# Kernel optimization log

Hardware: AMD Instinct MI355X
Metric: run time of the kernel (lower is better)

## Reference

```python
import jax, jax.numpy as jnp
import numpy as np

B, H, T, K, V = 2, 8, 2048, 128, 128


def setup_inputs() -> dict:
    key = jax.random.key(0)
    k1, k2, k3, k4, k5 = jax.random.split(key, 5)
    return {
        "q": jax.random.normal(k1, (B, H, T, K), dtype=jnp.float32),
        "k": jax.random.normal(k2, (B, H, T, K), dtype=jnp.float32),
        "v": jax.random.normal(k3, (B, H, T, V), dtype=jnp.float32),
        "i_gate": jax.random.normal(k4, (B, H, T), dtype=jnp.float32),
        "f_gate": jax.random.normal(k5, (B, H, T), dtype=jnp.float32),
    }


def reference(q, k, v, i_gate, f_gate):
    # Stabilized parallel mLSTM (same math as the chunked Triton kernel,
    # expressed in natural-log base instead of base-2).
    Bq, Hq, Tq, Kd = q.shape
    scale = Kd ** -0.5
    logf = jax.nn.log_sigmoid(f_gate)                      # [B,H,T]
    fc = jnp.cumsum(logf, axis=-1)                         # cumulative forget logits
    # log decay matrix: logD[t,s] = i[s] + (fc[t] - fc[s]) for s <= t
    logD = fc[..., :, None] - fc[..., None, :] + i_gate[..., None, :]  # [B,H,T,T]
    mask = jnp.tril(jnp.ones((Tq, Tq), dtype=bool))
    logD_masked = jnp.where(mask, logD, -jnp.inf)
    m = jnp.max(logD_masked, axis=-1)                      # row-wise stabilizer [B,H,T]
    D = jnp.where(mask, jnp.exp(logD - m[..., None]), 0.0) # stabilized decay matrix
    S = jnp.einsum("bhtk,bhsk->bhts", q, k) * scale * D    # gated scores
    norm = jnp.maximum(jnp.abs(jnp.sum(S, axis=-1)), jnp.exp(-m))  # [B,H,T]
    h = jnp.einsum("bhts,bhsv->bhtv", S, v) / norm[..., None]
    return h
```

## Files before the change

kernel.cpp:

```cpp
#include <hip/hip_runtime.h>

#define T_SEQ 2048
#define DHEAD 128
#define NBH 16
#define SCALE 0.08838834764831845f

typedef unsigned short u16;
typedef u16 u16x4 __attribute__((ext_vector_type(4)));
typedef u16 u16x8 __attribute__((ext_vector_type(8)));
typedef __bf16 bf16x8 __attribute__((ext_vector_type(8)));
typedef float f32x4 __attribute__((ext_vector_type(4)));

__device__ __forceinline__ u16 f2bfu(float x) {
  union { float f; unsigned u; } c; c.f = x;
  unsigned u = c.u;
  u = u + 0x7FFFu + ((u >> 16) & 1u);
  return (u16)(u >> 16);
}

__device__ __forceinline__ bf16x8 ldsFrag(const u16* p) {
  u16x8 t = *(const u16x8*)p;
  return __builtin_bit_cast(bf16x8, t);
}

__device__ __forceinline__ void gld_lds16(const void* g, void* l) {
  __builtin_amdgcn_global_load_lds(
      (__attribute__((address_space(1))) const unsigned int*)g,
      (__attribute__((address_space(3))) unsigned int*)l, 16, 0, 0);
}

__global__ __launch_bounds__(256) void gate_scan_kernel(
    const float* __restrict__ ig, const float* __restrict__ fg,
    float* __restrict__ a_out, float* __restrict__ c_out,
    float* __restrict__ nfl_out)
{
  const int bh  = blockIdx.x;
  const int tid = threadIdx.x;
  const int base = bh * T_SEQ + tid * 8;
  __shared__ float sbuf[256];

  float lf[8];
  float run = 0.f;
#pragma unroll
  for (int j = 0; j < 8; ++j) {
    float x  = fg[base + j];
    float ls = fminf(x, 0.f) - log1pf(expf(-fabsf(x)));
    run += ls; lf[j] = run;
  }
  sbuf[tid] = run; __syncthreads();
  for (int off = 1; off < 256; off <<= 1) {
    float t = (tid >= off) ? sbuf[tid - off] : 0.f;
    __syncthreads();
    sbuf[tid] += t;
    __syncthreads();
  }
  const float excl = (tid > 0) ? sbuf[tid - 1] : 0.f;
  __syncthreads();

  float fc[8], cm[8];
  float runm = -INFINITY;
#pragma unroll
  for (int j = 0; j < 8; ++j) {
    fc[j] = excl + lf[j];
    float av = ig[base + j] - fc[j];
    a_out[base + j] = av;
    runm = fmaxf(runm, av);
    cm[j] = runm;
  }
  sbuf[tid] = runm; __syncthreads();
  for (int off = 1; off < 256; off <<= 1) {
    float t = (tid >= off) ? sbuf[tid - off] : -INFINITY;
    __syncthreads();
    sbuf[tid] = fmaxf(sbuf[tid], t);
    __syncthreads();
  }
  const float exclm = (tid > 0) ? sbuf[tid - 1] : -INFINITY;
#pragma unroll
  for (int j = 0; j < 8; ++j) {
    float c = fmaxf(exclm, cm[j]);
    c_out[base + j]   = c;
    nfl_out[base + j] = expf(-(c + fc[j]));
  }
}

__global__ __launch_bounds__(256) void cvt_k_kernel(
    const float* __restrict__ src, u16* __restrict__ dst)
{
  const int i = (blockIdx.x * 256 + threadIdx.x) * 4;
  const float4 x = *(const float4*)(src + i);
  u16x4 p; p[0] = f2bfu(x.x); p[1] = f2bfu(x.y); p[2] = f2bfu(x.z); p[3] = f2bfu(x.w);
  *(u16x4*)(dst + i) = p;
}

__global__ __launch_bounds__(256) void cvt_vt_kernel(
    const float* __restrict__ v, u16* __restrict__ vt)
{
  const int bh = blockIdx.y, kt = blockIdx.x, tid = threadIdx.x;
  __shared__ __align__(16) u16 L[128 * 72];
  const int n0 = (tid & 31) * 4, k0 = (tid >> 5) * 8;
  const float* vp = v + ((size_t)bh * T_SEQ + kt * 64 + k0) * DHEAD + n0;
  u16 tv[4][8];
#pragma unroll
  for (int rr = 0; rr < 8; ++rr) {
    const float4 x = *(const float4*)(vp + rr * DHEAD);
    tv[0][rr] = f2bfu(x.x); tv[1][rr] = f2bfu(x.y);
    tv[2][rr] = f2bfu(x.z); tv[3][rr] = f2bfu(x.w);
  }
#pragma unroll
  for (int j = 0; j < 4; ++j) {
    u16x8 p;
#pragma unroll
    for (int rr = 0; rr < 8; ++rr) p[rr] = tv[j][rr];
    *(u16x8*)(&L[(n0 + j) * 72 + k0]) = p;
  }
  __syncthreads();
  const int row = tid >> 1, s0 = (tid & 1) * 32;
  u16* op = vt + ((size_t)bh * DHEAD + row) * T_SEQ + kt * 64 + s0;
#pragma unroll
  for (int i = 0; i < 4; ++i)
    *(u16x8*)(op + i * 8) = *(const u16x8*)(&L[row * 72 + s0 + i * 8]);
}

template <bool FAST>
__global__ __launch_bounds__(256, 2) void mlstm_fwd_kernel(
    const float* __restrict__ qg, const float* __restrict__ kg,
    const float* __restrict__ vg,
    const u16* __restrict__ kbf, const u16* __restrict__ vtbf,
    const float* __restrict__ ag, const float* __restrict__ cg,
    const float* __restrict__ nflg, float* __restrict__ out)
{
  const int bx = (int)blockIdx.x;
  const int xs = bx & 7, js = bx >> 3;
  const int bh = xs + 8 * (js & 1);
  const int qt = 31 - (js >> 1);

  const int tid  = (int)threadIdx.x;
  const int wave = tid >> 6, lane = tid & 63;
  const int quad = lane >> 4, l16 = lane & 15;

  __shared__ __align__(16) u16 KB[2][64 * 128];
  __shared__ __align__(16) u16 VB[2][128 * 64];
  __shared__ __align__(16) u16 Pl[4][16 * 72];

  const size_t hoff = (size_t)bh * T_SEQ * DHEAD;
  const int goff = bh * T_SEQ;
  const int qrowA = qt * 64 + wave * 16 + l16;
  const int trow0 = qt * 64 + wave * 16 + quad * 4;

  bf16x8 qf[4];
  {
    const float* qp = qg + hoff + (size_t)qrowA * DHEAD + quad * 8;
#pragma unroll
    for (int kc = 0; kc < 4; ++kc) {
      const float4 x0 = *(const float4*)(qp + kc * 32);
      const float4 x1 = *(const float4*)(qp + kc * 32 + 4);
      u16x8 t;
      t[0] = f2bfu(x0.x); t[1] = f2bfu(x0.y); t[2] = f2bfu(x0.z); t[3] = f2bfu(x0.w);
      t[4] = f2bfu(x1.x); t[5] = f2bfu(x1.y); t[6] = f2bfu(x1.z); t[7] = f2bfu(x1.w);
      qf[kc] = __builtin_bit_cast(bf16x8, t);
    }
  }
  float cr[4];
#pragma unroll
  for (int r = 0; r < 4; ++r) cr[r] = cg[goff + trow0 + r];

  f32x4 oa[8];
#pragma unroll
  for (int nv = 0; nv < 8; ++nv) oa[nv] = (f32x4){0.f, 0.f, 0.f, 0.f};
  float rs[4] = {0.f, 0.f, 0.f, 0.f};

  float4 kr[8], vr[8];
  const int fb_keyb = tid >> 4;
  const int fb_db   = (tid & 15) ^ ((tid >> 4) & 7);
  const int fb_n0 = (tid & 31) * 4, fb_k0 = (tid >> 5) * 8;

  auto stage_issue = [&](int kt, int b) {
    if (FAST) {
      const u16* ks = kbf + ((size_t)goff + kt * 64) * DHEAD;
      const u16* vs = vtbf + (size_t)bh * DHEAD * T_SEQ + kt * 64;
#pragma unroll
      for (int j = 0; j < 4; ++j) {
        const int B = (wave * 4 + j) * 64 + lane;
        {
          const int key = B >> 4;
          const int db = (B & 15) ^ (key & 7);
          gld_lds16(ks + (size_t)key * DHEAD + db * 8, &KB[b][(wave * 4 + j) * 512]);
        }
        {
          const int n = B >> 3;
          const int kb = (B & 7) ^ (n & 7);
          gld_lds16(vs + (size_t)n * T_SEQ + kb * 8, &VB[b][(wave * 4 + j) * 512]);
        }
      }
    } else {
      const float* kp = kg + hoff + (size_t)(kt * 64) * DHEAD;
      const float* vp = vg + hoff + (size_t)(kt * 64 + fb_k0) * DHEAD + fb_n0;
#pragma unroll
      for (int jb = 0; jb < 4; ++jb) {
        const int key = fb_keyb + 16 * jb;
        kr[2 * jb]     = *(const float4*)(kp + (size_t)key * DHEAD + fb_db * 8);
        kr[2 * jb + 1] = *(const float4*)(kp + (size_t)key * DHEAD + fb_db * 8 + 4);
      }
#pragma unroll
      for (int rr = 0; rr < 8; ++rr) vr[rr] = *(const float4*)(vp + rr * DHEAD);
    }
  };
  auto stage_commit = [&](int b) {
    if (!FAST) {
#pragma unroll
      for (int jb = 0; jb < 4; ++jb) {
        const int key = fb_keyb + 16 * jb;
        u16x8 p;
        p[0] = f2bfu(kr[2*jb].x);   p[1] = f2bfu(kr[2*jb].y);
        p[2] = f2bfu(kr[2*jb].z);   p[3] = f2bfu(kr[2*jb].w);
        p[4] = f2bfu(kr[2*jb+1].x); p[5] = f2bfu(kr[2*jb+1].y);
        p[6] = f2bfu(kr[2*jb+1].z); p[7] = f2bfu(kr[2*jb+1].w);
        *(u16x8*)(&KB[b][(key * 16 + (tid & 15)) * 8]) = p;
      }
      u16 tv[4][8];
#pragma unroll
      for (int rr = 0; rr < 8; ++rr) {
        tv[0][rr] = f2bfu(vr[rr].x); tv[1][rr] = f2bfu(vr[rr].y);
        tv[2][rr] = f2bfu(vr[rr].z); tv[3][rr] = f2bfu(vr[rr].w);
      }
      const int kb = fb_k0 >> 3;
#pragma unroll
      for (int j = 0; j < 4; ++j) {
        const int n = fb_n0 + j;
        u16x8 p;
#pragma unroll
        for (int rr = 0; rr < 8; ++rr) p[rr] = tv[j][rr];
        *(u16x8*)(&VB[b][(n * 8 + (kb ^ (n & 7))) * 8]) = p;
      }
    }
  };

  stage_issue(0, 0);
  stage_commit(0);
  __syncthreads();

  for (int kt = 0; kt <= qt; ++kt) {
    const int b = kt & 1;
    if (kt < qt) stage_issue(kt + 1, b ^ 1);

    float an[4];
#pragma unroll
    for (int nc = 0; nc < 4; ++nc) an[nc] = ag[goff + kt * 64 + nc * 16 + l16];

    const bool diag = (kt == qt);
#pragma unroll
    for (int nc = 0; nc < 4; ++nc) {
      f32x4 s = (f32x4){0.f, 0.f, 0.f, 0.f};
      const int key = nc * 16 + l16;
#pragma unroll
      for (int kc = 0; kc < 4; ++kc) {
        const int db = (kc * 4 + quad) ^ (l16 & 7);
        const bf16x8 bk = ldsFrag(&KB[b][(key * 16 + db) * 8]);
        s = __builtin_amdgcn_mfma_f32_16x16x32_bf16(qf[kc], bk, s, 0, 0, 0);
      }
      const float asv = an[nc];
      const int scol = nc * 16 + l16;
#pragma unroll
      for (int r = 0; r < 4; ++r) {
        float p = s[r] * (SCALE * __expf(asv - cr[r]));
        if (diag && (kt * 64 + scol > trow0 + r)) p = 0.f;
        rs[r] += p;
        Pl[wave][(quad * 4 + r) * 72 + scol] = f2bfu(p);
      }
    }
#pragma unroll
    for (int kk = 0; kk < 2; ++kk) {
      const bf16x8 pa = ldsFrag(&Pl[wave][l16 * 72 + kk * 32 + quad * 8]);
#pragma unroll
      for (int nv = 0; nv < 8; ++nv) {
        const int n = nv * 16 + l16;
        const int kb = (kk * 4 + quad) ^ (l16 & 7);
        const bf16x8 bv = ldsFrag(&VB[b][(n * 8 + kb) * 8]);
        oa[nv] = __builtin_amdgcn_mfma_f32_16x16x32_bf16(pa, bv, oa[nv], 0, 0, 0);
      }
    }
    if (kt < qt) stage_commit(b ^ 1);
    __syncthreads();
  }

#pragma unroll
  for (int r = 0; r < 4; ++r) {
    float x = rs[r];
#pragma unroll
    for (int off = 1; off < 16; off <<= 1) x += __shfl_xor(x, off, 64);
    rs[r] = x;
  }
  float inv[4];
#pragma unroll
  for (int r = 0; r < 4; ++r) {
    const float nf = nflg[goff + trow0 + r];
    inv[r] = 1.f / fmaxf(fabsf(rs[r]), nf);
  }
  float* op = out + hoff;
#pragma unroll
  for (int nv = 0; nv < 8; ++nv) {
#pragma unroll
    for (int r = 0; r < 4; ++r) {
      op[(size_t)(trow0 + r) * DHEAD + nv * 16 + l16] = oa[nv][r] * inv[r];
    }
  }
}

extern "C" void kernel_launch(void* const* d_in, const int* in_sizes, int n_in,
                              void* d_out, int out_size, void* d_ws, size_t ws_size,
                              hipStream_t stream) {
  const float* q  = (const float*)d_in[0];
  const float* k  = (const float*)d_in[1];
  const float* v  = (const float*)d_in[2];
  const float* ig = (const float*)d_in[3];
  const float* fg = (const float*)d_in[4];

  const size_t gate_bytes = (size_t)3 * NBH * T_SEQ * sizeof(float);
  const size_t kv_elems   = (size_t)NBH * T_SEQ * DHEAD;
  const bool fast = ws_size >= gate_bytes + 2 * kv_elems * sizeof(u16);

  float* a_ws   = (float*)d_ws;
  float* c_ws   = a_ws + NBH * T_SEQ;
  float* nfl_ws = c_ws + NBH * T_SEQ;
  u16* kbf  = (u16*)((char*)d_ws + gate_bytes);
  u16* vtbf = kbf + kv_elems;

  gate_scan_kernel<<<dim3(NBH), dim3(256), 0, stream>>>(ig, fg, a_ws, c_ws, nfl_ws);
  if (fast) {
    cvt_k_kernel<<<dim3((unsigned)(kv_elems / 1024)), dim3(256), 0, stream>>>(k, kbf);
    cvt_vt_kernel<<<dim3(T_SEQ / 64, NBH), dim3(256), 0, stream>>>(v, vtbf);
    mlstm_fwd_kernel<true><<<dim3(512), dim3(256), 0, stream>>>(
        q, k, v, kbf, vtbf, a_ws, c_ws, nfl_ws, (float*)d_out);
  } else {
    mlstm_fwd_kernel<false><<<dim3(512), dim3(256), 0, stream>>>(
        q, k, v, kbf, vtbf, a_ws, c_ws, nfl_ws, (float*)d_out);
  }
}
```

Measured before the change: 154.5 us.

## Pair complementary query tiles per block and hoist exp stabilizer per tile

Each 512-thread block now handles two query tiles of the same head, p and 31-p, in two 256-thread groups. This gives every block the same causal work, and the 256-block grid can place one block per CU. The per-element exp(a - c_row) is replaced by a per-column exp(a - c_tile) and a per-row correction at the end, which cuts exponentials in the inner loop. The P scratch tile gets an XOR swizzle to reduce LDS bank conflicts. Costs: the two groups load K/V separately, so traffic is duplicated, and the shorter group idles at barriers until the longer one finishes. The new stabilization also carries some overflow and precision risk.

Result: slower. 158.0 us (+2.2%).

```diff
diff --git a/kernel.cpp b/kernel.cpp
--- a/kernel.cpp
+++ b/kernel.cpp
@@ -122,7 +122,7 @@
 }
 
 template <bool FAST>
-__global__ __launch_bounds__(256, 2) void mlstm_fwd_kernel(
+__global__ __launch_bounds__(512, 1) void mlstm_fwd_kernel(
     const float* __restrict__ qg, const float* __restrict__ kg,
     const float* __restrict__ vg,
     const u16* __restrict__ kbf, const u16* __restrict__ vtbf,
@@ -130,17 +130,20 @@
     const float* __restrict__ nflg, float* __restrict__ out)
 {
   const int bx = (int)blockIdx.x;
-  const int xs = bx & 7, js = bx >> 3;
-  const int bh = xs + 8 * (js & 1);
-  const int qt = 31 - (js >> 1);
-
-  const int tid  = (int)threadIdx.x;
-  const int wave = tid >> 6, lane = tid & 63;
+  const int bh = bx & 15, p = bx >> 4;
+  const int tid = (int)threadIdx.x;
+  const int grp = tid >> 8;
+  const int gt  = tid & 255;
+  const int wave = gt >> 6, lane = gt & 63;
   const int quad = lane >> 4, l16 = lane & 15;
-
-  __shared__ __align__(16) u16 KB[2][64 * 128];
-  __shared__ __align__(16) u16 VB[2][128 * 64];
-  __shared__ __align__(16) u16 Pl[4][16 * 72];
+  const int w8   = tid >> 6;
+
+  const int qt    = grp ? p : (31 - p);
+  const int qtMax = 31 - p;
+
+  __shared__ __align__(16) u16 KB[2][2][64 * 128];
+  __shared__ __align__(16) u16 VB[2][2][128 * 64];
+  __shared__ __align__(16) u16 Pl[8][16 * 64];
 
   const size_t hoff = (size_t)bh * T_SEQ * DHEAD;
   const int goff = bh * T_SEQ;
@@ -160,9 +163,7 @@
       qf[kc] = __builtin_bit_cast(bf16x8, t);
     }
   }
-  float cr[4];
-#pragma unroll
-  for (int r = 0; r < 4; ++r) cr[r] = cg[goff + trow0 + r];
+  const float cmax = cg[goff + qt * 64 + 63];
 
   f32x4 oa[8];
 #pragma unroll
@@ -170,9 +171,9 @@
   float rs[4] = {0.f, 0.f, 0.f, 0.f};
 
   float4 kr[8], vr[8];
-  const int fb_keyb = tid >> 4;
-  const int fb_db   = (tid & 15) ^ ((tid >> 4) & 7);
-  const int fb_n0 = (tid & 31) * 4, fb_k0 = (tid >> 5) * 8;
+  const int fb_keyb = gt >> 4;
+  const int fb_db   = (gt & 15) ^ ((gt >> 4) & 7);
+  const int fb_n0 = (gt & 31) * 4, fb_k0 = (gt >> 5) * 8;
 
   auto stage_issue = [&](int kt, int b) {
     if (FAST) {
@@ -184,12 +185,12 @@
         {
           const int key = B >> 4;
           const int db = (B & 15) ^ (key & 7);
-          gld_lds16(ks + (size_t)key * DHEAD + db * 8, &KB[b][(wave * 4 + j) * 512]);
+          gld_lds16(ks + (size_t)key * DHEAD + db * 8, &KB[grp][b][(wave * 4 + j) * 512]);
         }
         {
           const int n = B >> 3;
           const int kb = (B & 7) ^ (n & 7);
-          gld_lds16(vs + (size_t)n * T_SEQ + kb * 8, &VB[b][(wave * 4 + j) * 512]);
+          gld_lds16(vs + (size_t)n * T_SEQ + kb * 8, &VB[grp][b][(wave * 4 + j) * 512]);
         }
       }
     } else {
@@ -210,12 +211,12 @@
 #pragma unroll
       for (int jb = 0; jb < 4; ++jb) {
         const int key = fb_keyb + 16 * jb;
-        u16x8 p;
-        p[0] = f2bfu(kr[2*jb].x);   p[1] = f2bfu(kr[2*jb].y);
-        p[2] = f2bfu(kr[2*jb].z);   p[3] = f2bfu(kr[2*jb].w);
-        p[4] = f2bfu(kr[2*jb+1].x); p[5] = f2bfu(kr[2*jb+1].y);
-        p[6] = f2bfu(kr[2*jb+1].z); p[7] = f2bfu(kr[2*jb+1].w);
-        *(u16x8*)(&KB[b][(key * 16 + (tid & 15)) * 8]) = p;
+        u16x8 pk;
+        pk[0] = f2bfu(kr[2*jb].x);   pk[1] = f2bfu(kr[2*jb].y);
+        pk[2] = f2bfu(kr[2*jb].z);   pk[3] = f2bfu(kr[2*jb].w);
+        pk[4] = f2bfu(kr[2*jb+1].x); pk[5] = f2bfu(kr[2*jb+1].y);
+        pk[6] = f2bfu(kr[2*jb+1].z); pk[7] = f2bfu(kr[2*jb+1].w);
+        *(u16x8*)(&KB[grp][b][(key * 16 + (gt & 15)) * 8]) = pk;
       }
       u16 tv[4][8];
 #pragma unroll
@@ -227,10 +228,10 @@
 #pragma unroll
       for (int j = 0; j < 4; ++j) {
         const int n = fb_n0 + j;
-        u16x8 p;
-#pragma unroll
-        for (int rr = 0; rr < 8; ++rr) p[rr] = tv[j][rr];
-        *(u16x8*)(&VB[b][(n * 8 + (kb ^ (n & 7))) * 8]) = p;
+        u16x8 pk;
+#pragma unroll
+        for (int rr = 0; rr < 8; ++rr) pk[rr] = tv[j][rr];
+        *(u16x8*)(&VB[grp][b][(n * 8 + (kb ^ (n & 7))) * 8]) = pk;
       }
     }
   };
@@ -239,47 +240,51 @@
   stage_commit(0);
   __syncthreads();
 
-  for (int kt = 0; kt <= qt; ++kt) {
+  for (int kt = 0; kt <= qtMax; ++kt) {
     const int b = kt & 1;
-    if (kt < qt) stage_issue(kt + 1, b ^ 1);
-
-    float an[4];
-#pragma unroll
-    for (int nc = 0; nc < 4; ++nc) an[nc] = ag[goff + kt * 64 + nc * 16 + l16];
-
-    const bool diag = (kt == qt);
-#pragma unroll
-    for (int nc = 0; nc < 4; ++nc) {
-      f32x4 s = (f32x4){0.f, 0.f, 0.f, 0.f};
-      const int key = nc * 16 + l16;
-#pragma unroll
-      for (int kc = 0; kc < 4; ++kc) {
-        const int db = (kc * 4 + quad) ^ (l16 & 7);
-        const bf16x8 bk = ldsFrag(&KB[b][(key * 16 + db) * 8]);
-        s = __builtin_amdgcn_mfma_f32_16x16x32_bf16(qf[kc], bk, s, 0, 0, 0);
-      }
-      const float asv = an[nc];
-      const int scol = nc * 16 + l16;
-#pragma unroll
-      for (int r = 0; r < 4; ++r) {
-        float p = s[r] * (SCALE * __expf(asv - cr[r]));
-        if (diag && (kt * 64 + scol > trow0 + r)) p = 0.f;
-        rs[r] += p;
-        Pl[wave][(quad * 4 + r) * 72 + scol] = f2bfu(p);
-      }
-    }
-#pragma unroll
-    for (int kk = 0; kk < 2; ++kk) {
-      const bf16x8 pa = ldsFrag(&Pl[wave][l16 * 72 + kk * 32 + quad * 8]);
-#pragma unroll
-      for (int nv = 0; nv < 8; ++nv) {
-        const int n = nv * 16 + l16;
-        const int kb = (kk * 4 + quad) ^ (l16 & 7);
-        const bf16x8 bv = ldsFrag(&VB[b][(n * 8 + kb) * 8]);
-        oa[nv] = __builtin_amdgcn_mfma_f32_16x16x32_bf16(pa, bv, oa[nv], 0, 0, 0);
-      }
-    }
-    if (kt < qt) stage_commit(b ^ 1);
+    const bool act = (kt <= qt);
+    if (act && kt < qt) stage_issue(kt + 1, b ^ 1);
+
+    if (act) {
+      float an[4];
+#pragma unroll
+      for (int nc = 0; nc < 4; ++nc) an[nc] = ag[goff + kt * 64 + nc * 16 + l16];
+
+      const bool diag = (kt == qt);
+#pragma unroll
+      for (int nc = 0; nc < 4; ++nc) {
+        f32x4 s = (f32x4){0.f, 0.f, 0.f, 0.f};
+        const int key = nc * 16 + l16;
+#pragma unroll
+        for (int kc = 0; kc < 4; ++kc) {
+          const int db = (kc * 4 + quad) ^ (l16 & 7);
+          const bf16x8 bk = ldsFrag(&KB[grp][b][(key * 16 + db) * 8]);
+          s = __builtin_amdgcn_mfma_f32_16x16x32_bf16(qf[kc], bk, s, 0, 0, 0);
+        }
+        const float es = SCALE * __expf(an[nc] - cmax);
+        const int scol = nc * 16 + l16;
+#pragma unroll
+        for (int r = 0; r < 4; ++r) {
+          float pv = s[r] * es;
+          if (diag && (kt * 64 + scol > trow0 + r)) pv = 0.f;
+          rs[r] += pv;
+          const int m = quad * 4 + r;
+          Pl[w8][m * 64 + ((((scol >> 3) ^ (m & 7)) << 3) | (scol & 7))] = f2bfu(pv);
+        }
+      }
+#pragma unroll
+      for (int kk = 0; kk < 2; ++kk) {
+        const bf16x8 pa = ldsFrag(&Pl[w8][l16 * 64 + (((kk * 4 + quad) ^ (l16 & 7)) << 3)]);
+#pragma unroll
+        for (int nv = 0; nv < 8; ++nv) {
+          const int n = nv * 16 + l16;
+          const int kb = (kk * 4 + quad) ^ (l16 & 7);
+          const bf16x8 bv = ldsFrag(&VB[grp][b][(n * 8 + kb) * 8]);
+          oa[nv] = __builtin_amdgcn_mfma_f32_16x16x32_bf16(pa, bv, oa[nv], 0, 0, 0);
+        }
+      }
+    }
+    if (act && kt < qt) stage_commit(b ^ 1);
     __syncthreads();
   }
 
@@ -293,8 +298,10 @@
   float inv[4];
 #pragma unroll
   for (int r = 0; r < 4; ++r) {
-    const float nf = nflg[goff + trow0 + r];
-    inv[r] = 1.f / fmaxf(fabsf(rs[r]), nf);
+    const float crv  = cg[goff + trow0 + r];
+    const float erow = __expf(cmax - crv);
+    const float nf   = nflg[goff + trow0 + r];
+    inv[r] = erow / fmaxf(fabsf(rs[r] * erow), nf);
   }
   float* op = out + hoff;
 #pragma unroll
@@ -329,10 +336,10 @@
   if (fast) {
     cvt_k_kernel<<<dim3((unsigned)(kv_elems / 1024)), dim3(256), 0, stream>>>(k, kbf);
     cvt_vt_kernel<<<dim3(T_SEQ / 64, NBH), dim3(256), 0, stream>>>(v, vtbf);
-    mlstm_fwd_kernel<true><<<dim3(512), dim3(256), 0, stream>>>(
+    mlstm_fwd_kernel<true><<<dim3(256), dim3(512), 0, stream>>>(
         q, k, v, kbf, vtbf, a_ws, c_ws, nfl_ws, (float*)d_out);
   } else {
-    mlstm_fwd_kernel<false><<<dim3(512), dim3(256), 0, stream>>>(
+    mlstm_fwd_kernel<false><<<dim3(256), dim3(512), 0, stream>>>(
         q, k, v, kbf, vtbf, a_ws, c_ws, nfl_ws, (float*)d_out);
   }
 }
```
